# Kernel tuning notes

Measured on AMD Instinct MI355X. Metric: run time of the kernel, lower is better.

The kernel has to match this reference:

```python
import jax, jax.numpy as jnp
import numpy as np

L, H, D, HD, DFF, V, S, B = 12, 12, 768, 64, 3072, 50257, 512, 4
NEG = -1e10  # mask value used by the torch module (applied incl. diagonal, pre-scale)


def layer_norm(x, g, b, eps=1e-5):
    u = jnp.mean(x, axis=-1, keepdims=True)
    v = jnp.mean((x - u) ** 2, axis=-1, keepdims=True)  # biased variance
    return g * (x - u) / jnp.sqrt(v + eps) + b


def setup_inputs() -> dict:
    key = jax.random.key(0)
    ks = jax.random.split(key, 10)
    f = lambda k, s: 0.02 * jax.random.normal(k, s, dtype=jnp.float32)
    return {
        "tokens": jax.random.randint(ks[0], (B, S), 0, V),
        "E": f(ks[1], (V, D)),
        "P": f(ks[2], (S, D)),
        "Wq": f(ks[3], (L, H, HD, D)),
        "Wk": f(ks[4], (L, H, HD, D)),
        "Wv": f(ks[5], (L, H, HD, D)),
        "Wo": f(ks[6], (L, D, D)),
        "bo": jnp.zeros((L, D), jnp.float32),
        "g1": jnp.ones((L, D), jnp.float32),
        "b1": jnp.zeros((L, D), jnp.float32),
        "g2": jnp.ones((L, D), jnp.float32),
        "b2": jnp.zeros((L, D), jnp.float32),
        "W1": f(ks[7], (L, DFF, D)),
        "bff1": jnp.zeros((L, DFF), jnp.float32),
        "W2": f(ks[8], (L, D, DFF)),
        "bff2": jnp.zeros((L, D), jnp.float32),
        "gf": jnp.ones((D,), jnp.float32),
        "bf": jnp.zeros((D,), jnp.float32),
    }


def reference(tokens, E, P, Wq, Wk, Wv, Wo, bo, g1, b1, g2, b2, W1, bff1, W2, bff2, gf, bf):
    x = E[tokens] + P[None, :, :]  # [B,S,D]; embed_dropout is identity at eval
    # Faithful mask: triu with diagonal=0 (masks the diagonal too), added BEFORE 1/sqrt(dk)
    mask = jnp.triu(jnp.ones((S, S), jnp.float32), k=0) * NEG
    scale = 1.0 / jnp.sqrt(jnp.float32(HD))
    for l in range(L):
        h = layer_norm(x, g1[l], b1[l])
        Q = jnp.einsum('bsd,hkd->bhsk', h, Wq[l])
        K = jnp.einsum('bsd,hkd->bhsk', h, Wk[l])
        Vh = jnp.einsum('bsd,hkd->bhsk', h, Wv[l])
        sc = (jnp.einsum('bhqk,bhmk->bhqm', Q, K) + mask) * scale  # [B,H,S,S]
        A = jax.nn.softmax(sc, axis=-1)
        o = jnp.einsum('bhqm,bhmk->bhqk', A, Vh)  # [B,H,S,HD]
        o = o.transpose(0, 2, 1, 3).reshape(B, S, D)  # concat heads
        x = x + jnp.einsum('bsd,ed->bse', o, Wo[l]) + bo[l]
        h2 = layer_norm(x, g2[l], b2[l])
        ff = jax.nn.gelu(jnp.einsum('bsd,fd->bsf', h2, W1[l]) + bff1[l], approximate=False)
        x = x + jnp.einsum('bsf,df->bsd', ff, W2[l]) + bff2[l]
    x = layer_norm(x, gf, bf)
    return jnp.einsum('bsd,vd->bsv', x, E)  # weight-tied LM head
```

## Files before the change

### kernel.cpp

```cpp
#include <hip/hip_runtime.h>
#include <hip/hip_bf16.h>
#include <math.h>
#include <stdint.h>

#define L      12
#define H      12
#define DMODEL 768
#define HDIM   64
#define DFF    3072
#define VOCAB  50257
#define VPAD2  50432
#define SEQ    512
#define BATCH  4
#define MTOK   2048

typedef __hip_bfloat16 bf16;
typedef __bf16 bf16x8 __attribute__((ext_vector_type(8)));
typedef float  f32x4  __attribute__((ext_vector_type(4)));

__device__ inline float bfbits2f(unsigned int u) {
    return __builtin_bit_cast(float, u << 16);
}
__device__ inline unsigned int f2bf_bits(float f) {
    __hip_bfloat16 h = __float2bfloat16(f);
    return (unsigned int)__builtin_bit_cast(unsigned short, h);
}

typedef __attribute__((address_space(1))) unsigned int as1_uint;
typedef __attribute__((address_space(3))) unsigned int as3_uint;

__device__ inline void load_lds_16B(const void* g, void* l) {
    __builtin_amdgcn_global_load_lds((as1_uint*)(uintptr_t)g,
                                     (as3_uint*)(uintptr_t)l, 16, 0, 0);
}

__device__ inline int xcd_swz(int raw, int nwg) {
    return (raw & 7) * (nwg >> 3) + (raw >> 3);
}

__global__ void cvt_pad_kernel(bf16* __restrict__ dst, const float* __restrict__ src,
                               long ns, long nt) {
    long i8 = ((long)blockIdx.x * blockDim.x + threadIdx.x) * 8;
    long stride = (long)gridDim.x * blockDim.x * 8;
    for (; i8 < nt; i8 += stride) {
        uint4 out;
        if (i8 < ns) {
            float4 a = *reinterpret_cast<const float4*>(src + i8);
            float4 b = *reinterpret_cast<const float4*>(src + i8 + 4);
            out.x = f2bf_bits(a.x) | (f2bf_bits(a.y) << 16);
            out.y = f2bf_bits(a.z) | (f2bf_bits(a.w) << 16);
            out.z = f2bf_bits(b.x) | (f2bf_bits(b.y) << 16);
            out.w = f2bf_bits(b.z) | (f2bf_bits(b.w) << 16);
        } else {
            out = (uint4){0u, 0u, 0u, 0u};
        }
        *reinterpret_cast<uint4*>(dst + i8) = out;
    }
}

__global__ __launch_bounds__(256) void embed_ln_kernel(
        float* __restrict__ x, bf16* __restrict__ hout,
        const int* __restrict__ tok, const float* __restrict__ E,
        const float* __restrict__ P, const float* __restrict__ g,
        const float* __restrict__ b) {
    int wave = threadIdx.x >> 6, lane = threadIdx.x & 63;
    int row = blockIdx.x * 4 + wave;
    int s = row & (SEQ - 1);
    long ebase = (long)tok[row] * 192;
    const float4* E4 = (const float4*)E;
    const float4* P4 = (const float4*)P;
    float4 v[3];
    float s1 = 0.f, s2 = 0.f;
    #pragma unroll
    for (int e = 0; e < 3; e++) {
        int c4 = e * 64 + lane;
        float4 a = E4[ebase + c4];
        float4 p = P4[s * 192 + c4];
        a.x += p.x; a.y += p.y; a.z += p.z; a.w += p.w;
        v[e] = a;
        ((float4*)x)[(size_t)row * 192 + c4] = a;
        s1 += a.x + a.y + a.z + a.w;
        s2 += a.x * a.x + a.y * a.y + a.z * a.z + a.w * a.w;
    }
    #pragma unroll
    for (int o = 32; o > 0; o >>= 1) {
        s1 += __shfl_xor(s1, o);
        s2 += __shfl_xor(s2, o);
    }
    float u    = s1 * (1.f / DMODEL);
    float var  = s2 * (1.f / DMODEL) - u * u;
    float rstd = rsqrtf(var + 1e-5f);
    #pragma unroll
    for (int e = 0; e < 3; e++) {
        int c4 = e * 64 + lane;
        float4 gg = ((const float4*)g)[c4];
        float4 bb = ((const float4*)b)[c4];
        float y0 = gg.x * (v[e].x - u) * rstd + bb.x;
        float y1 = gg.y * (v[e].y - u) * rstd + bb.y;
        float y2 = gg.z * (v[e].z - u) * rstd + bb.z;
        float y3 = gg.w * (v[e].w - u) * rstd + bb.w;
        uint2 o2;
        o2.x = f2bf_bits(y0) | (f2bf_bits(y1) << 16);
        o2.y = f2bf_bits(y2) | (f2bf_bits(y3) << 16);
        ((uint2*)hout)[(size_t)row * 192 + c4] = o2;
    }
}

__global__ __launch_bounds__(256) void reduce_ln_kernel(
        float* __restrict__ x, const float* __restrict__ part, int S,
        const float* __restrict__ bias, const float* __restrict__ g,
        const float* __restrict__ b, bf16* __restrict__ hout) {
    int wave = threadIdx.x >> 6, lane = threadIdx.x & 63;
    int row = blockIdx.x * 4 + wave;
    const float4* part4 = (const float4*)part;
    float4 v[3];
    float s1 = 0.f, s2 = 0.f;
    #pragma unroll
    for (int e = 0; e < 3; e++) {
        int c4 = e * 64 + lane;
        size_t idx = (size_t)row * 192 + c4;
        float4 a = ((const float4*)x)[idx];
        float4 bi = ((const float4*)bias)[c4];
        a.x += bi.x; a.y += bi.y; a.z += bi.z; a.w += bi.w;
        for (int sl = 0; sl < S; sl++) {
            float4 p = part4[((size_t)sl * MTOK + row) * 192 + c4];
            a.x += p.x; a.y += p.y; a.z += p.z; a.w += p.w;
        }
        v[e] = a;
        ((float4*)x)[idx] = a;
        s1 += a.x + a.y + a.z + a.w;
        s2 += a.x * a.x + a.y * a.y + a.z * a.z + a.w * a.w;
    }
    #pragma unroll
    for (int o = 32; o > 0; o >>= 1) {
        s1 += __shfl_xor(s1, o);
        s2 += __shfl_xor(s2, o);
    }
    float u    = s1 * (1.f / DMODEL);
    float var  = s2 * (1.f / DMODEL) - u * u;
    float rstd = rsqrtf(var + 1e-5f);
    #pragma unroll
    for (int e = 0; e < 3; e++) {
        int c4 = e * 64 + lane;
        float4 gg = ((const float4*)g)[c4];
        float4 bb = ((const float4*)b)[c4];
        float y0 = gg.x * (v[e].x - u) * rstd + bb.x;
        float y1 = gg.y * (v[e].y - u) * rstd + bb.y;
        float y2 = gg.z * (v[e].z - u) * rstd + bb.z;
        float y3 = gg.w * (v[e].w - u) * rstd + bb.w;
        uint2 o2;
        o2.x = f2bf_bits(y0) | (f2bf_bits(y1) << 16);
        o2.y = f2bf_bits(y2) | (f2bf_bits(y3) << 16);
        ((uint2*)hout)[(size_t)row * 192 + c4] = o2;
    }
}

#define BM 128
#define BKK 64

template<int BN_, int EPI>
__global__ __launch_bounds__(256) void gemm_bt(
    const bf16* __restrict__ A, const bf16* __restrict__ Bmat, long strideBz,
    void* __restrict__ Cout, long strideCz,
    const float* __restrict__ bias,
    int Mm, int Nn, int Kk, int Nstore, int kslice)
{
    constexpr int NF = BN_ / 32;
    __shared__ __align__(16) bf16 As[2][BM * BKK];
    __shared__ __align__(16) bf16 Bs[2][BN_ * BKK];
    int tid = threadIdx.x;
    int lane = tid & 63, wave = tid >> 6;

    int Mtiles = Mm / BM;
    int id = xcd_swz(blockIdx.x, gridDim.x);
    int bm = (id % Mtiles) * BM;
    int bn = (id / Mtiles) * BN_;
    int z = blockIdx.z;
    const bf16* Bz = Bmat + (size_t)z * strideBz;
    int wr = (wave >> 1) * 64, wc = (wave & 1) * (BN_ / 2);

    int k0 = (EPI == 4) ? z * kslice : 0;
    int nt = ((EPI == 4) ? kslice : Kk) / BKK;

    f32x4 acc[4][NF];
    #pragma unroll
    for (int i = 0; i < 4; i++)
        #pragma unroll
        for (int j = 0; j < NF; j++) acc[i][j] = (f32x4){0.f, 0.f, 0.f, 0.f};

    auto stage = [&](int slot, int kt) {
        #pragma unroll
        for (int i = 0; i < 4; i++) {
            int byte = i * 4096 + tid * 16;
            int r = byte >> 7;
            int scb = (byte & 127) ^ ((r & 7) << 4);
            load_lds_16B(A + (size_t)(bm + r) * Kk + kt + (scb >> 1),
                         (char*)As[slot] + byte);
        }
        #pragma unroll
        for (int i = 0; i < BN_ / 32; i++) {
            int byte = i * 4096 + tid * 16;
            int r = byte >> 7;
            int scb = (byte & 127) ^ ((r & 7) << 4);
            load_lds_16B(Bz + (size_t)(bn + r) * Kk + kt + (scb >> 1),
                         (char*)Bs[slot] + byte);
        }
    };

    const int swz_rd = (lane & 7) << 4;
    auto compute = [&](int cur) {
        #pragma unroll
        for (int kk = 0; kk < 2; ++kk) {
            bf16x8 af[4], bfr[NF];
            int ro = lane & 15;
            int cob = kk * 64 + (lane >> 4) * 16;
            #pragma unroll
            for (int mi = 0; mi < 4; mi++) {
                int row = wr + mi * 16 + ro;
                af[mi] = *reinterpret_cast<const bf16x8*>(
                    (const char*)As[cur] + row * 128 + (cob ^ swz_rd));
            }
            #pragma unroll
            for (int ni = 0; ni < NF; ni++) {
                int row = wc + ni * 16 + ro;
                bfr[ni] = *reinterpret_cast<const bf16x8*>(
                    (const char*)Bs[cur] + row * 128 + (cob ^ swz_rd));
            }
            #pragma unroll
            for (int mi = 0; mi < 4; mi++)
                #pragma unroll
                for (int ni = 0; ni < NF; ni++)
                    acc[mi][ni] = __builtin_amdgcn_mfma_f32_16x16x32_bf16(
                        af[mi], bfr[ni], acc[mi][ni], 0, 0, 0);
        }
    };

    stage(0, k0);
    for (int t = 0; t < nt; ++t) {
        if (t + 1 < nt) {
            stage((t + 1) & 1, k0 + (t + 1) * BKK);
            if constexpr (BN_ == 128) {
                asm volatile("s_waitcnt vmcnt(8)" ::: "memory");
            } else {
                asm volatile("s_waitcnt vmcnt(6)" ::: "memory");
            }
        } else {
            asm volatile("s_waitcnt vmcnt(0)" ::: "memory");
        }
        __builtin_amdgcn_s_barrier();
        __builtin_amdgcn_sched_barrier(0);
        __builtin_amdgcn_s_setprio(1);
        compute(t & 1);
        __builtin_amdgcn_s_setprio(0);
        __builtin_amdgcn_s_barrier();
    }

    int rbase = bm + wr + ((lane >> 4) << 2);
    int cbase = bn + wc + (lane & 15);
    #pragma unroll
    for (int mi = 0; mi < 4; mi++) {
        #pragma unroll
        for (int ni = 0; ni < NF; ni++) {
            int col = cbase + ni * 16;
            #pragma unroll
            for (int r = 0; r < 4; r++) {
                int row = rbase + mi * 16 + r;
                float v = acc[mi][ni][r];
                if constexpr (EPI == 0) {
                    ((bf16*)Cout)[(size_t)z * strideCz + (size_t)row * Nn + col] =
                        __float2bfloat16(v);
                } else if constexpr (EPI == 2) {
                    float t = v + bias[col];
                    float gel = 0.5f * t * (1.f + erff(t * 0.70710678118654752f));
                    ((bf16*)Cout)[(size_t)row * Nn + col] = __float2bfloat16(gel);
                } else if constexpr (EPI == 3) {
                    if (col < Nstore)
                        ((float*)Cout)[(size_t)row * Nstore + col] = v;
                } else {
                    ((float*)Cout)[(size_t)z * strideCz + (size_t)row * Nn + col] = v;
                }
            }
        }
    }
}

#define NEGMASK -1e10f
#define SM_SCALE 0.125f

__global__ __launch_bounds__(256) void attn_kernel(
    bf16* __restrict__ o, const bf16* __restrict__ qb,
    const bf16* __restrict__ kb, const bf16* __restrict__ vb)
{
    __shared__ __align__(16) bf16 K_lds[64 * 64];
    __shared__ __align__(16) bf16 VT_lds[64 * 64];
    __shared__ __align__(16) bf16 P_lds[4][16 * 64];

    int tid = threadIdx.x;
    int wave = tid >> 6, lane = tid & 63;
    int g = lane >> 4;
    int cq = lane & 15;
    int idx = xcd_swz(blockIdx.x, gridDim.x);
    int qt = idx & 7;
    int bh = idx >> 3;
    int h = bh % H, b = bh / H;
    int q0 = qt * 64;
    const size_t base = ((size_t)b * SEQ) * DMODEL + h * HDIM;

    bf16x8 qa[2];
    #pragma unroll
    for (int kk = 0; kk < 2; kk++)
        qa[kk] = *reinterpret_cast<const bf16x8*>(
            qb + base + (size_t)(q0 + wave * 16 + cq) * DMODEL + kk * 32 + g * 8);

    f32x4 acc_o[4];
    #pragma unroll
    for (int df = 0; df < 4; df++) acc_o[df] = (f32x4){0.f, 0.f, 0.f, 0.f};
    float m_run[4] = {-INFINITY, -INFINITY, -INFINITY, -INFINITY};
    float l_run[4] = {0.f, 0.f, 0.f, 0.f};

    int ntiles = (qt == 0) ? (SEQ / 64) : (qt + 1);
    for (int t = 0; t < ntiles; ++t) {
        int mt = t * 64;
        __syncthreads();
        #pragma unroll
        for (int i = 0; i < 2; i++) {
            int byte = i * 4096 + tid * 16;
            int r = byte >> 7;
            int scb = (byte & 127) ^ ((r & 7) << 4);
            load_lds_16B(kb + base + (size_t)(mt + r) * DMODEL + (scb >> 1),
                         (char*)K_lds + byte);
        }
        {
            int rp = tid & 31;
            int c0 = (tid >> 5) * 8;
            const bf16* v0p = vb + base + (size_t)(mt + 2 * rp) * DMODEL + c0;
            uint4 a = *reinterpret_cast<const uint4*>(v0p);
            uint4 bb = *reinterpret_cast<const uint4*>(v0p + DMODEL);
            unsigned int au[4] = {a.x, a.y, a.z, a.w};
            unsigned int bu[4] = {bb.x, bb.y, bb.z, bb.w};
            #pragma unroll
            for (int j = 0; j < 8; j++) {
                unsigned int lo = (j & 1) ? (au[j >> 1] >> 16) : (au[j >> 1] & 0xffffu);
                unsigned int hi = (j & 1) ? (bu[j >> 1] >> 16) : (bu[j >> 1] & 0xffffu);
                int d = c0 + j;
                int byte = d * 128 + ((rp * 4) ^ ((d & 7) << 4));
                *reinterpret_cast<unsigned int*>((char*)VT_lds + byte) = lo | (hi << 16);
            }
        }
        __syncthreads();

        f32x4 s[4];
        #pragma unroll
        for (int nf = 0; nf < 4; nf++) s[nf] = (f32x4){0.f, 0.f, 0.f, 0.f};
        __builtin_amdgcn_s_setprio(1);
        #pragma unroll
        for (int kk = 0; kk < 2; kk++) {
            #pragma unroll
            for (int nf = 0; nf < 4; nf++) {
                int row = nf * 16 + cq;
                bf16x8 kf = *reinterpret_cast<const bf16x8*>(
                    (const char*)K_lds + row * 128 +
                    ((kk * 64 + g * 16) ^ ((row & 7) << 4)));
                s[nf] = __builtin_amdgcn_mfma_f32_16x16x32_bf16(qa[kk], kf, s[nf], 0, 0, 0);
            }
        }
        __builtin_amdgcn_s_setprio(0);

        float p[4][4];
        #pragma unroll
        for (int r = 0; r < 4; r++) {
            int qg = q0 + wave * 16 + (g << 2) + r;
            float sv[4];
            float vmax = -INFINITY;
            #pragma unroll
            for (int nf = 0; nf < 4; nf++) {
                int kv = mt + nf * 16 + cq;
                float d = s[nf][r];
                sv[nf] = (kv >= qg) ? (d + NEGMASK) * SM_SCALE : d * SM_SCALE;
                vmax = fmaxf(vmax, sv[nf]);
            }
            vmax = fmaxf(vmax, __shfl_xor(vmax, 1));
            vmax = fmaxf(vmax, __shfl_xor(vmax, 2));
            vmax = fmaxf(vmax, __shfl_xor(vmax, 4));
            vmax = fmaxf(vmax, __shfl_xor(vmax, 8));
            float nm = fmaxf(m_run[r], vmax);
            float f = __expf(m_run[r] - nm);
            m_run[r] = nm;
            float ps = 0.f;
            #pragma unroll
            for (int nf = 0; nf < 4; nf++) {
                float pv = __expf(sv[nf] - nm);
                p[nf][r] = pv;
                ps += pv;
            }
            ps += __shfl_xor(ps, 1);
            ps += __shfl_xor(ps, 2);
            ps += __shfl_xor(ps, 4);
            ps += __shfl_xor(ps, 8);
            l_run[r] = l_run[r] * f + ps;
            #pragma unroll
            for (int df = 0; df < 4; df++) acc_o[df][r] *= f;
        }

        #pragma unroll
        for (int nf = 0; nf < 4; nf++)
            #pragma unroll
            for (int r = 0; r < 4; r++) {
                int q = (g << 2) + r;
                int blog = nf * 32 + cq * 2;
                int byte = wave * 2048 + q * 128 + (blog ^ ((q & 7) << 4));
                *reinterpret_cast<unsigned short*>((char*)P_lds + byte) =
                    (unsigned short)f2bf_bits(p[nf][r]);
            }
        __syncthreads();

        __builtin_amdgcn_s_setprio(1);
        #pragma unroll
        for (int kk = 0; kk < 2; kk++) {
            bf16x8 pa = *reinterpret_cast<const bf16x8*>(
                (const char*)P_lds + wave * 2048 + cq * 128 +
                ((kk * 64 + g * 16) ^ ((cq & 7) << 4)));
            #pragma unroll
            for (int df = 0; df < 4; df++) {
                int row = df * 16 + cq;
                bf16x8 vf = *reinterpret_cast<const bf16x8*>(
                    (const char*)VT_lds + row * 128 +
                    ((kk * 64 + g * 16) ^ ((row & 7) << 4)));
                acc_o[df] = __builtin_amdgcn_mfma_f32_16x16x32_bf16(pa, vf, acc_o[df], 0, 0, 0);
            }
        }
        __builtin_amdgcn_s_setprio(0);
    }

    #pragma unroll
    for (int r = 0; r < 4; r++) {
        float inv = 1.f / l_run[r];
        int qg = q0 + wave * 16 + (g << 2) + r;
        #pragma unroll
        for (int df = 0; df < 4; df++) {
            o[base + (size_t)qg * DMODEL + df * 16 + cq] =
                __float2bfloat16(acc_o[df][r] * inv);
        }
    }
}

extern "C" void kernel_launch(void* const* d_in, const int* in_sizes, int n_in,
                              void* d_out, int out_size, void* d_ws, size_t ws_size,
                              hipStream_t stream)
{
    (void)in_sizes; (void)n_in; (void)out_size; (void)ws_size;
    const int*   tokens = (const int*)d_in[0];
    const float* E    = (const float*)d_in[1];
    const float* P    = (const float*)d_in[2];
    const float* Wq   = (const float*)d_in[3];
    const float* Wk   = (const float*)d_in[4];
    const float* Wv   = (const float*)d_in[5];
    const float* Wo   = (const float*)d_in[6];
    const float* bo   = (const float*)d_in[7];
    const float* g1   = (const float*)d_in[8];
    const float* b1   = (const float*)d_in[9];
    const float* g2   = (const float*)d_in[10];
    const float* b2   = (const float*)d_in[11];
    const float* W1   = (const float*)d_in[12];
    const float* bff1 = (const float*)d_in[13];
    const float* W2   = (const float*)d_in[14];
    const float* bff2 = (const float*)d_in[15];
    const float* gf   = (const float*)d_in[16];
    const float* bfin = (const float*)d_in[17];

    char* ws = (char*)d_ws;
    size_t off = 0;
    auto alloc = [&](size_t bytes) -> void* {
        void* p = ws + off;
        off += (bytes + 255) & ~(size_t)255;
        return p;
    };
    float* x     = (float*)alloc((size_t)MTOK * DMODEL * 4);
    bf16* hbuf   = (bf16*)alloc((size_t)MTOK * DMODEL * 2);
    bf16* qkv    = (bf16*)alloc((size_t)3 * MTOK * DMODEL * 2);
    bf16* obuf   = (bf16*)alloc((size_t)MTOK * DMODEL * 2);
    bf16* ffb    = (bf16*)alloc((size_t)MTOK * DFF * 2);
    float* part  = (float*)alloc((size_t)3 * MTOK * DMODEL * 4);
    bf16* Eb     = (bf16*)alloc((size_t)VPAD2 * DMODEL * 2);
    bf16* Wqkv_b = (bf16*)alloc((size_t)3 * L * DMODEL * DMODEL * 2);
    bf16* Wo_b   = (bf16*)alloc((size_t)L * DMODEL * DMODEL * 2);
    bf16* W1_b   = (bf16*)alloc((size_t)L * DFF * DMODEL * 2);
    bf16* W2_b   = (bf16*)alloc((size_t)L * DMODEL * DFF * 2);

    long nE  = (long)VOCAB * DMODEL;
    long nEp = (long)VPAD2 * DMODEL;
    cvt_pad_kernel<<<2048, 256, 0, stream>>>(Eb, E, nE, nEp);
    long nW = (long)L * DMODEL * DMODEL;
    cvt_pad_kernel<<<2048, 256, 0, stream>>>(Wqkv_b,          Wq, nW, nW);
    cvt_pad_kernel<<<2048, 256, 0, stream>>>(Wqkv_b + nW,     Wk, nW, nW);
    cvt_pad_kernel<<<2048, 256, 0, stream>>>(Wqkv_b + 2 * nW, Wv, nW, nW);
    cvt_pad_kernel<<<2048, 256, 0, stream>>>(Wo_b,            Wo, nW, nW);
    long nF = (long)L * DFF * DMODEL;
    cvt_pad_kernel<<<2048, 256, 0, stream>>>(W1_b, W1, nF, nF);
    cvt_pad_kernel<<<2048, 256, 0, stream>>>(W2_b, W2, nF, nF);

    embed_ln_kernel<<<MTOK / 4, 256, 0, stream>>>(x, hbuf, tokens, E, P, g1, b1);

    const long pstride = (long)MTOK * DMODEL;
    for (int l = 0; l < L; ++l) {
        gemm_bt<64, 0><<<dim3(16 * 12, 1, 3), 256, 0, stream>>>(
            hbuf, Wqkv_b + (size_t)l * DMODEL * DMODEL, (long)L * DMODEL * DMODEL,
            qkv, pstride, nullptr, MTOK, DMODEL, DMODEL, 0, 0);
        attn_kernel<<<BATCH * H * (SEQ / 64), 256, 0, stream>>>(
            obuf, qkv, qkv + pstride, qkv + 2 * pstride);
        gemm_bt<64, 4><<<dim3(16 * 12, 1, 3), 256, 0, stream>>>(
            obuf, Wo_b + (size_t)l * DMODEL * DMODEL, 0,
            part, pstride, nullptr, MTOK, DMODEL, DMODEL, 0, DMODEL / 3);
        reduce_ln_kernel<<<MTOK / 4, 256, 0, stream>>>(
            x, part, 3, bo + l * DMODEL, g2 + l * DMODEL, b2 + l * DMODEL, hbuf);
        gemm_bt<128, 2><<<dim3(16 * 24, 1, 1), 256, 0, stream>>>(
            hbuf, W1_b + (size_t)l * DFF * DMODEL, 0,
            ffb, 0, bff1 + l * DFF, MTOK, DFF, DMODEL, 0, 0);
        gemm_bt<64, 4><<<dim3(16 * 12, 1, 3), 256, 0, stream>>>(
            ffb, W2_b + (size_t)l * DMODEL * DFF, 0,
            part, pstride, nullptr, MTOK, DMODEL, DFF, 0, DFF / 3);
        const float* ng = (l < L - 1) ? (g1 + (l + 1) * DMODEL) : gf;
        const float* nb = (l < L - 1) ? (b1 + (l + 1) * DMODEL) : bfin;
        reduce_ln_kernel<<<MTOK / 4, 256, 0, stream>>>(
            x, part, 3, bff2 + l * DMODEL, ng, nb, hbuf);
    }
    gemm_bt<128, 3><<<dim3(16 * 394, 1, 1), 256, 0, stream>>>(
        hbuf, Eb, 0, d_out, 0, nullptr, MTOK, VPAD2, DMODEL, VOCAB, 0);
}
```

Measured before the change: 1.731 ms.

## Drop split-K for Wo/W2 and fuse residual+bias into GEMM epilogue

The Wo and W2 projection GEMMs no longer split K three ways into fp32 partial buffers. They now run a single K pass whose epilogue adds bias and the GEMM result directly into the fp32 residual x. The reduce+LayerNorm kernel becomes a plain LayerNorm that only reads x, which removes the partial-buffer writes and reads. The seven weight conversion launches are also merged into one kernel. In exchange, the Wo and W2 GEMMs launch only 192 workgroups, fewer than the number of CUs, and each W2 block runs a long K loop, which lowers occupancy.

```diff
diff --git a/kernel.cpp b/kernel.cpp
--- a/kernel.cpp
+++ b/kernel.cpp
@@ -13,14 +13,12 @@
 #define SEQ    512
 #define BATCH  4
 #define MTOK   2048
+#define BKK    64
 
 typedef __hip_bfloat16 bf16;
 typedef __bf16 bf16x8 __attribute__((ext_vector_type(8)));
 typedef float  f32x4  __attribute__((ext_vector_type(4)));
 
-__device__ inline float bfbits2f(unsigned int u) {
-    return __builtin_bit_cast(float, u << 16);
-}
 __device__ inline unsigned int f2bf_bits(float f) {
     __hip_bfloat16 h = __float2bfloat16(f);
     return (unsigned int)__builtin_bit_cast(unsigned short, h);
@@ -38,37 +36,48 @@
     return (raw & 7) * (nwg >> 3) + (raw >> 3);
 }
 
-__global__ void cvt_pad_kernel(bf16* __restrict__ dst, const float* __restrict__ src,
-                               long ns, long nt) {
-    long i8 = ((long)blockIdx.x * blockDim.x + threadIdx.x) * 8;
-    long stride = (long)gridDim.x * blockDim.x * 8;
-    for (; i8 < nt; i8 += stride) {
-        uint4 out;
-        if (i8 < ns) {
-            float4 a = *reinterpret_cast<const float4*>(src + i8);
-            float4 b = *reinterpret_cast<const float4*>(src + i8 + 4);
-            out.x = f2bf_bits(a.x) | (f2bf_bits(a.y) << 16);
-            out.y = f2bf_bits(a.z) | (f2bf_bits(a.w) << 16);
-            out.z = f2bf_bits(b.x) | (f2bf_bits(b.y) << 16);
-            out.w = f2bf_bits(b.z) | (f2bf_bits(b.w) << 16);
-        } else {
-            out = (uint4){0u, 0u, 0u, 0u};
-        }
-        *reinterpret_cast<uint4*>(dst + i8) = out;
+struct CvtP {
+    const float* src[7];
+    bf16* dst[7];
+    long ns[7];
+    long nt[7];
+};
+
+__global__ void cvt_all_kernel(CvtP c) {
+    long gid0 = ((long)blockIdx.x * blockDim.x + threadIdx.x) * 8;
+    long gstr = (long)gridDim.x * blockDim.x * 8;
+    for (int s = 0; s < 7; s++) {
+        const float* src = c.src[s];
+        bf16* dst = c.dst[s];
+        long ns = c.ns[s], ntt = c.nt[s];
+        for (long i8 = gid0; i8 < ntt; i8 += gstr) {
+            uint4 out;
+            if (i8 < ns) {
+                float4 a = *reinterpret_cast<const float4*>(src + i8);
+                float4 b = *reinterpret_cast<const float4*>(src + i8 + 4);
+                out.x = f2bf_bits(a.x) | (f2bf_bits(a.y) << 16);
+                out.y = f2bf_bits(a.z) | (f2bf_bits(a.w) << 16);
+                out.z = f2bf_bits(b.x) | (f2bf_bits(b.y) << 16);
+                out.w = f2bf_bits(b.z) | (f2bf_bits(b.w) << 16);
+            } else {
+                out = (uint4){0u, 0u, 0u, 0u};
+            }
+            *reinterpret_cast<uint4*>(dst + i8) = out;
+        }
     }
 }
 
 __global__ __launch_bounds__(256) void embed_ln_kernel(
         float* __restrict__ x, bf16* __restrict__ hout,
         const int* __restrict__ tok, const float* __restrict__ E,
-        const float* __restrict__ P, const float* __restrict__ g,
+        const float* __restrict__ Pp, const float* __restrict__ g,
         const float* __restrict__ b) {
     int wave = threadIdx.x >> 6, lane = threadIdx.x & 63;
     int row = blockIdx.x * 4 + wave;
     int s = row & (SEQ - 1);
     long ebase = (long)tok[row] * 192;
     const float4* E4 = (const float4*)E;
-    const float4* P4 = (const float4*)P;
+    const float4* P4 = (const float4*)Pp;
     float4 v[3];
     float s1 = 0.f, s2 = 0.f;
     #pragma unroll
@@ -106,28 +115,18 @@
     }
 }
 
-__global__ __launch_bounds__(256) void reduce_ln_kernel(
-        float* __restrict__ x, const float* __restrict__ part, int S,
-        const float* __restrict__ bias, const float* __restrict__ g,
+__global__ __launch_bounds__(256) void ln_kernel(
+        const float* __restrict__ x, const float* __restrict__ g,
         const float* __restrict__ b, bf16* __restrict__ hout) {
     int wave = threadIdx.x >> 6, lane = threadIdx.x & 63;
     int row = blockIdx.x * 4 + wave;
-    const float4* part4 = (const float4*)part;
     float4 v[3];
     float s1 = 0.f, s2 = 0.f;
     #pragma unroll
     for (int e = 0; e < 3; e++) {
         int c4 = e * 64 + lane;
-        size_t idx = (size_t)row * 192 + c4;
-        float4 a = ((const float4*)x)[idx];
-        float4 bi = ((const float4*)bias)[c4];
-        a.x += bi.x; a.y += bi.y; a.z += bi.z; a.w += bi.w;
-        for (int sl = 0; sl < S; sl++) {
-            float4 p = part4[((size_t)sl * MTOK + row) * 192 + c4];
-            a.x += p.x; a.y += p.y; a.z += p.z; a.w += p.w;
-        }
+        float4 a = ((const float4*)x)[(size_t)row * 192 + c4];
         v[e] = a;
-        ((float4*)x)[idx] = a;
         s1 += a.x + a.y + a.z + a.w;
         s2 += a.x * a.x + a.y * a.y + a.z * a.z + a.w * a.w;
     }
@@ -156,14 +155,13 @@
 }
 
 #define BM 128
-#define BKK 64
 
 template<int BN_, int EPI>
 __global__ __launch_bounds__(256) void gemm_bt(
     const bf16* __restrict__ A, const bf16* __restrict__ Bmat, long strideBz,
     void* __restrict__ Cout, long strideCz,
     const float* __restrict__ bias,
-    int Mm, int Nn, int Kk, int Nstore, int kslice)
+    int Mm, int Nn, int Kk, int Nstore)
 {
     constexpr int NF = BN_ / 32;
     __shared__ __align__(16) bf16 As[2][BM * BKK];
@@ -179,8 +177,7 @@
     const bf16* Bz = Bmat + (size_t)z * strideBz;
     int wr = (wave >> 1) * 64, wc = (wave & 1) * (BN_ / 2);
 
-    int k0 = (EPI == 4) ? z * kslice : 0;
-    int nt = ((EPI == 4) ? kslice : Kk) / BKK;
+    int nt = Kk / BKK;
 
     f32x4 acc[4][NF];
     #pragma unroll
@@ -208,7 +205,22 @@
     };
 
     const int swz_rd = (lane & 7) << 4;
-    auto compute = [&](int cur) {
+    stage(0, 0);
+    for (int t = 0; t < nt; ++t) {
+        if (t + 1 < nt) {
+            stage((t + 1) & 1, (t + 1) * BKK);
+            if constexpr (BN_ == 128) {
+                asm volatile("s_waitcnt vmcnt(8)" ::: "memory");
+            } else {
+                asm volatile("s_waitcnt vmcnt(6)" ::: "memory");
+            }
+        } else {
+            asm volatile("s_waitcnt vmcnt(0)" ::: "memory");
+        }
+        __builtin_amdgcn_s_barrier();
+        __builtin_amdgcn_sched_barrier(0);
+        __builtin_amdgcn_s_setprio(1);
+        int cur = t & 1;
         #pragma unroll
         for (int kk = 0; kk < 2; ++kk) {
             bf16x8 af[4], bfr[NF];
@@ -233,24 +245,6 @@
                     acc[mi][ni] = __builtin_amdgcn_mfma_f32_16x16x32_bf16(
                         af[mi], bfr[ni], acc[mi][ni], 0, 0, 0);
         }
-    };
-
-    stage(0, k0);
-    for (int t = 0; t < nt; ++t) {
-        if (t + 1 < nt) {
-            stage((t + 1) & 1, k0 + (t + 1) * BKK);
-            if constexpr (BN_ == 128) {
-                asm volatile("s_waitcnt vmcnt(8)" ::: "memory");
-            } else {
-                asm volatile("s_waitcnt vmcnt(6)" ::: "memory");
-            }
-        } else {
-            asm volatile("s_waitcnt vmcnt(0)" ::: "memory");
-        }
-        __builtin_amdgcn_s_barrier();
-        __builtin_amdgcn_sched_barrier(0);
-        __builtin_amdgcn_s_setprio(1);
-        compute(t & 1);
         __builtin_amdgcn_s_setprio(0);
         __builtin_amdgcn_s_barrier();
     }
@@ -269,15 +263,17 @@
                 if constexpr (EPI == 0) {
                     ((bf16*)Cout)[(size_t)z * strideCz + (size_t)row * Nn + col] =
                         __float2bfloat16(v);
+                } else if constexpr (EPI == 1) {
+                    size_t idx = (size_t)row * Nn + col;
+                    float* resid = (float*)Cout;
+                    resid[idx] = resid[idx] + v + bias[col];
                 } else if constexpr (EPI == 2) {
-                    float t = v + bias[col];
-                    float gel = 0.5f * t * (1.f + erff(t * 0.70710678118654752f));
+                    float t2 = v + bias[col];
+                    float gel = 0.5f * t2 * (1.f + erff(t2 * 0.70710678118654752f));
                     ((bf16*)Cout)[(size_t)row * Nn + col] = __float2bfloat16(gel);
-                } else if constexpr (EPI == 3) {
+                } else {
                     if (col < Nstore)
                         ((float*)Cout)[(size_t)row * Nstore + col] = v;
-                } else {
-                    ((float*)Cout)[(size_t)z * strideCz + (size_t)row * Nn + col] = v;
                 }
             }
         }
@@ -480,50 +476,48 @@
     bf16* qkv    = (bf16*)alloc((size_t)3 * MTOK * DMODEL * 2);
     bf16* obuf   = (bf16*)alloc((size_t)MTOK * DMODEL * 2);
     bf16* ffb    = (bf16*)alloc((size_t)MTOK * DFF * 2);
-    float* part  = (float*)alloc((size_t)3 * MTOK * DMODEL * 4);
     bf16* Eb     = (bf16*)alloc((size_t)VPAD2 * DMODEL * 2);
     bf16* Wqkv_b = (bf16*)alloc((size_t)3 * L * DMODEL * DMODEL * 2);
     bf16* Wo_b   = (bf16*)alloc((size_t)L * DMODEL * DMODEL * 2);
     bf16* W1_b   = (bf16*)alloc((size_t)L * DFF * DMODEL * 2);
     bf16* W2_b   = (bf16*)alloc((size_t)L * DMODEL * DFF * 2);
 
-    long nE  = (long)VOCAB * DMODEL;
-    long nEp = (long)VPAD2 * DMODEL;
-    cvt_pad_kernel<<<2048, 256, 0, stream>>>(Eb, E, nE, nEp);
     long nW = (long)L * DMODEL * DMODEL;
-    cvt_pad_kernel<<<2048, 256, 0, stream>>>(Wqkv_b,          Wq, nW, nW);
-    cvt_pad_kernel<<<2048, 256, 0, stream>>>(Wqkv_b + nW,     Wk, nW, nW);
-    cvt_pad_kernel<<<2048, 256, 0, stream>>>(Wqkv_b + 2 * nW, Wv, nW, nW);
-    cvt_pad_kernel<<<2048, 256, 0, stream>>>(Wo_b,            Wo, nW, nW);
     long nF = (long)L * DFF * DMODEL;
-    cvt_pad_kernel<<<2048, 256, 0, stream>>>(W1_b, W1, nF, nF);
-    cvt_pad_kernel<<<2048, 256, 0, stream>>>(W2_b, W2, nF, nF);
+    CvtP cp;
+    cp.src[0] = E;  cp.dst[0] = Eb;          cp.ns[0] = (long)VOCAB * DMODEL; cp.nt[0] = (long)VPAD2 * DMODEL;
+    cp.src[1] = Wq; cp.dst[1] = Wqkv_b;      cp.ns[1] = nW; cp.nt[1] = nW;
+    cp.src[2] = Wk; cp.dst[2] = Wqkv_b + nW; cp.ns[2] = nW; cp.nt[2] = nW;
+    cp.src[3] = Wv; cp.dst[3] = Wqkv_b + 2 * nW; cp.ns[3] = nW; cp.nt[3] = nW;
+    cp.src[4] = Wo; cp.dst[4] = Wo_b;        cp.ns[4] = nW; cp.nt[4] = nW;
+    cp.src[5] = W1; cp.dst[5] = W1_b;        cp.ns[5] = nF; cp.nt[5] = nF;
+    cp.src[6] = W2; cp.dst[6] = W2_b;        cp.ns[6] = nF; cp.nt[6] = nF;
+    cvt_all_kernel<<<2048, 256, 0, stream>>>(cp);
 
     embed_ln_kernel<<<MTOK / 4, 256, 0, stream>>>(x, hbuf, tokens, E, P, g1, b1);
 
     const long pstride = (long)MTOK * DMODEL;
     for (int l = 0; l < L; ++l) {
-        gemm_bt<64, 0><<<dim3(16 * 12, 1, 3), 256, 0, stream>>>(
-            hbuf, Wqkv_b + (size_t)l * DMODEL * DMODEL, (long)L * DMODEL * DMODEL,
-            qkv, pstride, nullptr, MTOK, DMODEL, DMODEL, 0, 0);
+        gemm_bt<64, 0><<<dim3(192, 1, 3), 256, 0, stream>>>(
+            hbuf, Wqkv_b + (size_t)l * DMODEL * DMODEL, nW,
+            qkv, pstride, nullptr, MTOK, DMODEL, DMODEL, 0);
         attn_kernel<<<BATCH * H * (SEQ / 64), 256, 0, stream>>>(
             obuf, qkv, qkv + pstride, qkv + 2 * pstride);
-        gemm_bt<64, 4><<<dim3(16 * 12, 1, 3), 256, 0, stream>>>(
+        gemm_bt<64, 1><<<dim3(192, 1, 1), 256, 0, stream>>>(
             obuf, Wo_b + (size_t)l * DMODEL * DMODEL, 0,
-            part, pstride, nullptr, MTOK, DMODEL, DMODEL, 0, DMODEL / 3);
-        reduce_ln_kernel<<<MTOK / 4, 256, 0, stream>>>(
-            x, part, 3, bo + l * DMODEL, g2 + l * DMODEL, b2 + l * DMODEL, hbuf);
+            x, 0, bo + l * DMODEL, MTOK, DMODEL, DMODEL, 0);
+        ln_kernel<<<MTOK / 4, 256, 0, stream>>>(
+            x, g2 + l * DMODEL, b2 + l * DMODEL, hbuf);
         gemm_bt<128, 2><<<dim3(16 * 24, 1, 1), 256, 0, stream>>>(
             hbuf, W1_b + (size_t)l * DFF * DMODEL, 0,
-            ffb, 0, bff1 + l * DFF, MTOK, DFF, DMODEL, 0, 0);
-        gemm_bt<64, 4><<<dim3(16 * 12, 1, 3), 256, 0, stream>>>(
+            ffb, 0, bff1 + l * DFF, MTOK, DFF, DMODEL, 0);
+        gemm_bt<64, 1><<<dim3(192, 1, 1), 256, 0, stream>>>(
             ffb, W2_b + (size_t)l * DMODEL * DFF, 0,
-            part, pstride, nullptr, MTOK, DMODEL, DFF, 0, DFF / 3);
+            x, 0, bff2 + l * DMODEL, MTOK, DMODEL, DFF, 0);
         const float* ng = (l < L - 1) ? (g1 + (l + 1) * DMODEL) : gf;
         const float* nb = (l < L - 1) ? (b1 + (l + 1) * DMODEL) : bfin;
-        reduce_ln_kernel<<<MTOK / 4, 256, 0, stream>>>(
-            x, part, 3, bff2 + l * DMODEL, ng, nb, hbuf);
+        ln_kernel<<<MTOK / 4, 256, 0, stream>>>(x, ng, nb, hbuf);
     }
     gemm_bt<128, 3><<<dim3(16 * 394, 1, 1), 256, 0, stream>>>(
-        hbuf, Eb, 0, d_out, 0, nullptr, MTOK, VPAD2, DMODEL, VOCAB, 0);
-}
+        hbuf, Eb, 0, d_out, 0, nullptr, MTOK, VPAD2, DMODEL, VOCAB);
+}
```

Result: slower. 1.849 ms (+6.8%).
